# Kernel optimization log

Hardware: AMD Instinct MI355X
Metric: run time of the kernel (lower is better)

## Reference

```python
import jax, jax.numpy as jnp
import numpy as np
from jax import lax

B, C, H, W = 8, 256, 64, 64
A = 9                      # anchors per location (3 scales x 3 ratios)
STRIDE = 16
IMG = 1024                 # image_size
POST_NMS = 1000            # post_nms_top_n (also used as pre-NMS slice, as in source)
NMS_THR = 0.7
BBOX_XFORM_CLIP = 4.135166556742356  # log(1000/16)


def make_anchors():
    # ordering must match torch reshape (B,4,-1): index = a*H*W + h*W + w
    scales = jnp.array([128.0, 256.0, 512.0], dtype=jnp.float32)
    ratios = jnp.array([0.5, 1.0, 2.0], dtype=jnp.float32)
    ws = (scales[:, None] / jnp.sqrt(ratios)[None, :]).reshape(-1)  # [A]
    hs = (scales[:, None] * jnp.sqrt(ratios)[None, :]).reshape(-1)  # [A]
    cx = (jnp.arange(W, dtype=jnp.float32) + 0.5) * STRIDE
    cy = (jnp.arange(H, dtype=jnp.float32) + 0.5) * STRIDE
    cx = jnp.broadcast_to(cx[None, None, :], (A, H, W))
    cy = jnp.broadcast_to(cy[None, :, None], (A, H, W))
    aw = jnp.broadcast_to(ws[:, None, None], (A, H, W))
    ah = jnp.broadcast_to(hs[:, None, None], (A, H, W))
    anchors = jnp.stack([cx - aw / 2, cy - ah / 2, cx + aw / 2, cy + ah / 2], axis=-1)
    return anchors.reshape(-1, 4)  # [K,4] xyxy


def conv2d(x, w, b, pad):
    y = lax.conv_general_dilated(x, w, (1, 1), [(pad, pad), (pad, pad)],
                                 dimension_numbers=("NCHW", "OIHW", "NCHW"))
    return y + b[None, :, None, None]


def decode(t, anchors):
    # t: [K,4] (tx,ty,tw,th); anchors: [K,4] xyxy -> boxes xyxy
    aw = anchors[:, 2] - anchors[:, 0]
    ah = anchors[:, 3] - anchors[:, 1]
    acx = anchors[:, 0] + 0.5 * aw
    acy = anchors[:, 1] + 0.5 * ah
    cx = t[:, 0] * aw + acx
    cy = t[:, 1] * ah + acy
    w = jnp.exp(jnp.clip(t[:, 2], -BBOX_XFORM_CLIP, BBOX_XFORM_CLIP)) * aw
    h = jnp.exp(jnp.clip(t[:, 3], -BBOX_XFORM_CLIP, BBOX_XFORM_CLIP)) * ah
    return jnp.stack([cx - 0.5 * w, cy - 0.5 * h, cx + 0.5 * w, cy + 0.5 * h], axis=-1)


def box_iou(a, b):
    area_a = (a[:, 2] - a[:, 0]) * (a[:, 3] - a[:, 1])
    area_b = (b[:, 2] - b[:, 0]) * (b[:, 3] - b[:, 1])
    lt = jnp.maximum(a[:, None, :2], b[None, :, :2])
    rb = jnp.minimum(a[:, None, 2:], b[None, :, 2:])
    wh = jnp.clip(rb - lt, 0.0)
    inter = wh[..., 0] * wh[..., 1]
    return inter / (area_a[:, None] + area_b[None, :] - inter)


def filter_one(boxes, scores):
    # boxes [K,4], scores [K]. Faithful to source: torch.sort ascending,
    # slice to POST_NMS, then class-agnostic greedy NMS, pad to POST_NMS.
    order = jnp.argsort(lax.stop_gradient(scores))        # ascending (torch.sort default)
    idx = order[:POST_NMS]
    b = boxes[idx]
    s = scores[idx]
    # batched_nms internally processes boxes in descending-score order
    o2 = jnp.argsort(-lax.stop_gradient(s))
    b2 = b[o2]
    s2 = s[o2]
    iou = box_iou(b2, b2)  # [POST_NMS, POST_NMS]
    N = POST_NMS
    pos = jnp.arange(N)

    def body(i, keep):
        sup = (iou[i] > NMS_THR) & (pos > i) & keep[i]
        return keep & ~sup

    keep = lax.fori_loop(0, N, body, jnp.ones((N,), dtype=bool))
    # pack kept boxes (descending-score order) to the front, zero-pad the rest
    perm = jnp.argsort(jnp.where(keep, pos, N + pos))
    valid = pos < jnp.sum(keep)
    out_b = jnp.where(valid[:, None], b2[perm], 0.0)
    out_s = jnp.where(valid, s2[perm], 0.0)
    return out_b, out_s


def setup_inputs() -> dict:
    key = jax.random.key(0)
    ks = jax.random.split(key, 5)
    x = jax.random.normal(ks[0], (B, C, H, W), dtype=jnp.float32)
    conv_w = jax.random.normal(ks[1], (C, C, 3, 3), dtype=jnp.float32) * 0.01
    conv_b = jnp.zeros((C,), dtype=jnp.float32)
    box_w = jax.random.normal(ks[2], (4 * A, C, 1, 1), dtype=jnp.float32) * 0.01
    box_b = jnp.zeros((4 * A,), dtype=jnp.float32)
    obj_w = jax.random.normal(ks[3], (A, C, 1, 1), dtype=jnp.float32) * 0.01
    obj_b = jnp.zeros((A,), dtype=jnp.float32)
    return {"x": x, "conv_w": conv_w, "conv_b": conv_b,
            "box_w": box_w, "box_b": box_b, "obj_w": obj_w, "obj_b": obj_b}


def reference(x, conv_w, conv_b, box_w, box_b, obj_w, obj_b):
    feats = jax.nn.relu(conv2d(x, conv_w, conv_b, 1))        # [B,C,H,W]
    t = conv2d(feats, box_w, box_b, 0)                        # [B,4A,H,W]
    o = conv2d(feats, obj_w, obj_b, 0)                        # [B,A,H,W]
    t = t.reshape(B, 4, -1).transpose(0, 2, 1)                # [B,K,4]
    obj = o.reshape(B, -1)                                    # [B,K]
    anchors = make_anchors()                                  # [K,4]
    props = jax.vmap(lambda ti: decode(ti, anchors))(t)       # [B,K,4]
    props = jnp.clip(props, 0.0, float(IMG))                  # clip_boxes_to_image
    out_b, out_s = jax.vmap(filter_one)(props, obj)           # [B,POST_NMS,4],[B,POST_NMS]
    return jnp.concatenate([out_b, out_s[..., None]], axis=-1)  # [B,POST_NMS,5]
```

## Files before the change

kernel.cpp:

```cpp
#include <hip/hip_runtime.h>

#define B_ 8
#define C_ 256
#define H_ 64
#define W_ 64
#define HW_ 4096
#define HP_ 66
#define HWP_ 4224
#define A_ 9
#define SITES 36864
#define NPOST 1000
#define XCLIPF 4.1351666f
#define IMGF 1024.0f

__device__ inline unsigned keyf(float v) {
  unsigned u = __float_as_uint(v);
  return (u & 0x80000000u) ? ~u : (u | 0x80000000u);
}

__device__ __forceinline__ float dpp_shr1(float v) {
  return __int_as_float(__builtin_amdgcn_update_dpp(
      0, __float_as_int(v), 0x111 , 0xf, 0xf, true));
}
__device__ __forceinline__ float dpp_shl1(float v) {
  return __int_as_float(__builtin_amdgcn_update_dpp(
      0, __float_as_int(v), 0x101 , 0xf, 0xf, true));
}

__global__ __launch_bounds__(256) void prep(
    const float* __restrict__ x, const float* __restrict__ w,
    const float* __restrict__ box_w, const float* __restrict__ obj_w,
    float* __restrict__ xp, float* __restrict__ wq, float* __restrict__ wt) {
  int blk = blockIdx.x;
  if (blk < 8448) {
    int t = blk * 256 + threadIdx.x;
    int c4 = t & 15;
    int rr = (t >> 4) % HP_;
    int bc = t / (HP_ * 16);
    float4 v = make_float4(0.f, 0.f, 0.f, 0.f);
    if (rr >= 1 && rr <= 64)
      v = ((const float4*)x)[(size_t)bc * (HW_ / 4) + (size_t)(rr - 1) * 16 + c4];
    ((float4*)xp)[(size_t)bc * (HWP_ / 4) + (size_t)rr * 16 + c4] = v;
  } else if (blk < 8448 + 2304) {
    int idx = (blk - 8448) * 256 + threadIdx.x;
    int quad = idx / (256 * 36);
    int rem  = idx % (256 * 36);
    int ci = rem / 36;
    int k  = rem % 36;
    int q = k / 9, t = k % 9;
    wq[idx] = w[((size_t)(quad * 4 + q)) * (C_ * 9) + (size_t)ci * 9 + t];
  } else {
    int idx = (blk - 8448 - 2304) * 256 + threadIdx.x;
    if (idx < C_ * 45) {
      int ci = idx / 45, jj = idx % 45;
      wt[idx] = (jj < 36) ? box_w[(size_t)jj * C_ + ci]
                          : obj_w[(size_t)(jj - 36) * C_ + ci];
    }
  }
}

__global__ __launch_bounds__(256, 2) void conv3_4co(
    const float* __restrict__ xp, const float* __restrict__ wq,
    const float* __restrict__ bias, float* __restrict__ feats) {
#pragma clang fp contract(off)
  int b       = blockIdx.x & 7;
  int j       = blockIdx.x >> 3;
  int quad    = j & 63;
  int quarter = j >> 6;
  int co0 = quad << 2;
  int row16 = threadIdx.x >> 4;
  int chunk = threadIdx.x & 15;
  int gr = (quarter << 4) + row16;
  int c0 = chunk << 2;

  const float* px0 = xp + (size_t)b * C_ * HWP_ + (size_t)gr * W_ + c0;
  const float* wqb = wq + (size_t)quad * (C_ * 36);

  float acc[4][4][9];
#pragma unroll
  for (int q = 0; q < 4; ++q)
#pragma unroll
    for (int p = 0; p < 4; ++p)
#pragma unroll
      for (int t = 0; t < 9; ++t) acc[q][p][t] = 0.f;

#pragma unroll 2
  for (int ci = 0; ci < C_; ++ci) {
    const float* pr = px0 + (size_t)ci * HWP_;
    float4 tA = ((const float4*)(pr      ))[0];
    float4 mA = ((const float4*)(pr +  64))[0];
    float4 bA = ((const float4*)(pr + 128))[0];

    float T[6], M[6], Bo[6];
    T[1]=tA.x;  T[2]=tA.y;  T[3]=tA.z;  T[4]=tA.w;
    M[1]=mA.x;  M[2]=mA.y;  M[3]=mA.z;  M[4]=mA.w;
    Bo[1]=bA.x; Bo[2]=bA.y; Bo[3]=bA.z; Bo[4]=bA.w;

    T[0]  = dpp_shr1(T[4]);   T[5]  = dpp_shl1(T[1]);
    M[0]  = dpp_shr1(M[4]);   M[5]  = dpp_shl1(M[1]);
    Bo[0] = dpp_shr1(Bo[4]);  Bo[5] = dpp_shl1(Bo[1]);

    const float* wrow = wqb + ci * 36;
    float w9[4][9];
#pragma unroll
    for (int q = 0; q < 4; ++q)
#pragma unroll
      for (int t = 0; t < 9; ++t) w9[q][t] = wrow[q * 9 + t];

#pragma unroll
    for (int q = 0; q < 4; ++q)
#pragma unroll
      for (int p = 0; p < 4; ++p) {
        acc[q][p][0] = fmaf(w9[q][0], T[p],     acc[q][p][0]);
        acc[q][p][1] = fmaf(w9[q][1], T[p+1],   acc[q][p][1]);
        acc[q][p][2] = fmaf(w9[q][2], T[p+2],   acc[q][p][2]);
        acc[q][p][3] = fmaf(w9[q][3], M[p],     acc[q][p][3]);
        acc[q][p][4] = fmaf(w9[q][4], M[p+1],   acc[q][p][4]);
        acc[q][p][5] = fmaf(w9[q][5], M[p+2],   acc[q][p][5]);
        acc[q][p][6] = fmaf(w9[q][6], Bo[p],    acc[q][p][6]);
        acc[q][p][7] = fmaf(w9[q][7], Bo[p+1],  acc[q][p][7]);
        acc[q][p][8] = fmaf(w9[q][8], Bo[p+2],  acc[q][p][8]);
      }
  }

#pragma unroll
  for (int q = 0; q < 4; ++q) {
    float bv = bias[co0 + q];
    float ov[4];
#pragma unroll
    for (int p = 0; p < 4; ++p) {
      float a = 0.f;
#pragma unroll
      for (int t = 0; t < 9; ++t) a = a + acc[q][p][t];
      a = a + bv;
      ov[p] = a > 0.f ? a : 0.f;
    }
    float4* fo = (float4*)(feats + ((size_t)b * C_ + co0 + q) * HW_ + (size_t)gr * W_ + c0);
    fo[0] = make_float4(ov[0], ov[1], ov[2], ov[3]);
  }
}

__global__ __launch_bounds__(64) void conv1_all45(
    const float* __restrict__ feats, const float* __restrict__ wt,
    const float* __restrict__ box_b, const float* __restrict__ obj_b,
    float* __restrict__ tbox, float* __restrict__ scores) {
#pragma clang fp contract(off)
  int gidx = blockIdx.x * 64 + threadIdx.x;
  int b  = gidx >> 12;
  int hw = gidx & 4095;
  const float* f = feats + (size_t)b * C_ * HW_ + hw;
  float acc[45];
#pragma unroll
  for (int jj = 0; jj < 45; ++jj) acc[jj] = 0.f;
#pragma unroll 4
  for (int ci = 0; ci < C_; ++ci) {
    float fv = f[(size_t)ci * HW_];
    const float* wr = wt + ci * 45;
#pragma unroll
    for (int jj = 0; jj < 45; ++jj)
      acc[jj] = fmaf(wr[jj], fv, acc[jj]);
  }
#pragma unroll
  for (int c = 0; c < 36; ++c) {
    int k = c / 9, a = c - k * 9;
    tbox[(size_t)b * 4 * SITES + (size_t)k * SITES + (size_t)a * HW_ + hw] = acc[c] + box_b[c];
  }
#pragma unroll
  for (int a = 0; a < 9; ++a)
    scores[(size_t)b * SITES + (size_t)a * HW_ + hw] = acc[36 + a] + obj_b[a];
}

__global__ __launch_bounds__(1024) void select_sort_decode(
    const float* __restrict__ scores, const float* __restrict__ tbox,
    float* __restrict__ s2, float* __restrict__ b2) {
#pragma clang fp contract(off)
  int b = blockIdx.x;
  const float* s = scores + (size_t)b * SITES;
  __shared__ unsigned hist[256];
  __shared__ unsigned sh_prefix, sh_mask, sh_cless;
  __shared__ int sh_target;
  __shared__ int sh_cnt, sh_eq;
  __shared__ int sh_sel[1024];
  __shared__ int sh_eqList[4096];
  __shared__ float ss[NPOST];
  __shared__ int st[NPOST];
  if (threadIdx.x == 0) {
    sh_prefix = 0; sh_mask = 0; sh_target = NPOST - 1; sh_cless = 0;
    sh_cnt = 0; sh_eq = 0;
  }
  unsigned kreg[36];
#pragma unroll
  for (int t = 0; t < 36; ++t)
    kreg[t] = keyf(s[threadIdx.x + t * 1024]);
  for (int shift = 24; shift >= 0; shift -= 8) {
    if (threadIdx.x < 256) hist[threadIdx.x] = 0;
    __syncthreads();
    unsigned prefix = sh_prefix, mask = sh_mask;
#pragma unroll
    for (int t = 0; t < 36; ++t) {
      unsigned k = kreg[t];
      if ((k & mask) == prefix) atomicAdd(&hist[(k >> shift) & 255u], 1u);
    }
    __syncthreads();
    if (threadIdx.x == 0) {
      unsigned cum = 0; int tg = sh_target; int v = 0;
      for (; v < 256; ++v) {
        unsigned h = hist[v];
        if (cum + h > (unsigned)tg) break;
        cum += h;
      }
      sh_prefix |= ((unsigned)v) << shift;
      sh_mask   |= 0xFFu << shift;
      sh_target  = tg - (int)cum;
      sh_cless  += cum;
    }
    __syncthreads();
  }
  unsigned K = sh_prefix;
  int need = NPOST - (int)sh_cless;
#pragma unroll
  for (int t = 0; t < 36; ++t) {
    unsigned k = kreg[t];
    int i = threadIdx.x + t * 1024;
    if (k < K) {
      int pos = atomicAdd(&sh_cnt, 1);
      sh_sel[pos] = i;
    } else if (k == K) {
      int e = atomicAdd(&sh_eq, 1);
      if (e < 4096) sh_eqList[e] = i;
    }
  }
  __syncthreads();
  {
    int E = sh_eq; if (E > 4096) E = 4096;
    int base = sh_cnt;
    for (int t = threadIdx.x; t < E; t += 1024) {
      int site = sh_eqList[t];
      int rank = 0;
      for (int q = 0; q < E; ++q) rank += (sh_eqList[q] < site);
      if (rank < need) sh_sel[base + rank] = site;
    }
  }
  __syncthreads();
  for (int t = threadIdx.x; t < NPOST; t += 1024) {
    int site = sh_sel[t];
    st[t] = site;
    ss[t] = s[site];
  }
  __syncthreads();
  if (threadIdx.x < NPOST) {
    int r = threadIdx.x;
    float sr = ss[r]; int sir = st[r];
    int d = 0;
    for (int q = 0; q < NPOST; ++q) {
      float sq = ss[q];
      d += (int)((sq > sr) || (sq == sr && st[q] < sir));
    }
    s2[(size_t)b * NPOST + d] = sr;
    int site = sir;
    int a = site / HW_;
    int hw = site - a * HW_;
    int h = hw / W_, wc = hw - h * W_;
    int sidx = a / 3, ridx = a - sidx * 3;
    float scale = (sidx == 0) ? 128.f : ((sidx == 1) ? 256.f : 512.f);
    float ratio = (ridx == 0) ? 0.5f : ((ridx == 1) ? 1.0f : 2.0f);
    float sq = sqrtf(ratio);
    float wsa = scale / sq;
    float hsa = scale * sq;
    float cx = ((float)wc + 0.5f) * 16.f;
    float cy = ((float)h + 0.5f) * 16.f;
    float ax1 = cx - wsa * 0.5f;
    float ay1 = cy - hsa * 0.5f;
    float ax2 = cx + wsa * 0.5f;
    float ay2 = cy + hsa * 0.5f;
    float aw = ax2 - ax1, ah = ay2 - ay1;
    float m1 = 0.5f * aw, m2 = 0.5f * ah;
    float acx = ax1 + m1, acy = ay1 + m2;
    const float* tb = tbox + (size_t)b * 4 * SITES + site;
    float t0 = tb[0];
    float t1 = tb[SITES];
    float t2 = tb[2 * (size_t)SITES];
    float t3 = tb[3 * (size_t)SITES];
    if (t2 < -XCLIPF) t2 = -XCLIPF;
    if (t2 > XCLIPF) t2 = XCLIPF;
    if (t3 < -XCLIPF) t3 = -XCLIPF;
    if (t3 > XCLIPF) t3 = XCLIPF;
    float pm0 = t0 * aw;  float pcx = pm0 + acx;
    float pm1 = t1 * ah;  float pcy = pm1 + acy;
    float pw = expf(t2) * aw;
    float ph = expf(t3) * ah;
    float hw0 = 0.5f * pw, hh0 = 0.5f * ph;
    float x1 = pcx - hw0, y1 = pcy - hh0;
    float x2 = pcx + hw0, y2 = pcy + hh0;
    x1 = x1 < 0.f ? 0.f : (x1 > IMGF ? IMGF : x1);
    y1 = y1 < 0.f ? 0.f : (y1 > IMGF ? IMGF : y1);
    x2 = x2 < 0.f ? 0.f : (x2 > IMGF ? IMGF : x2);
    y2 = y2 < 0.f ? 0.f : (y2 > IMGF ? IMGF : y2);
    float* o = b2 + ((size_t)b * NPOST + d) * 4;
    o[0] = x1; o[1] = y1; o[2] = x2; o[3] = y2;
  }
}

__global__ __launch_bounds__(256) void mask_kernel(
    const float* __restrict__ b2, unsigned long long* __restrict__ sup) {
#pragma clang fp contract(off)
  int b = blockIdx.x / 63;
  int i0 = (blockIdx.x % 63) * 16;
  __shared__ float bs[NPOST * 4];
  __shared__ float area[NPOST];
  for (int t = threadIdx.x; t < NPOST * 4; t += 256) bs[t] = b2[(size_t)b * NPOST * 4 + t];
  __syncthreads();
  for (int t = threadIdx.x; t < NPOST; t += 256)
    area[t] = (bs[t * 4 + 2] - bs[t * 4]) * (bs[t * 4 + 3] - bs[t * 4 + 1]);
  __syncthreads();
  int i = i0 + (threadIdx.x & 15);
  int wd = threadIdx.x >> 4;
  if (i >= NPOST) return;
  float ax1 = bs[i * 4], ay1 = bs[i * 4 + 1], ax2 = bs[i * 4 + 2], ay2 = bs[i * 4 + 3];
  float aa = area[i];
  unsigned long long m = 0;
  for (int bit = 0; bit < 64; ++bit) {
    int j = wd * 64 + bit;
    if (j > i && j < NPOST) {
      float lx = fmaxf(ax1, bs[j * 4]);
      float ly = fmaxf(ay1, bs[j * 4 + 1]);
      float rx = fminf(ax2, bs[j * 4 + 2]);
      float ry = fminf(ay2, bs[j * 4 + 3]);
      float iw = rx - lx; if (iw < 0.f) iw = 0.f;
      float ih = ry - ly; if (ih < 0.f) ih = 0.f;
      float inter = iw * ih;
      float denom = (aa + area[j]) - inter;
      float iou = inter / denom;
      if (iou > 0.7f) m |= 1ull << bit;
    }
  }
  sup[((size_t)b * NPOST + i) * 16 + wd] = m;
}

__global__ __launch_bounds__(64) void nms_out(
    const unsigned long long* __restrict__ sup, const float* __restrict__ b2,
    const float* __restrict__ s2, float* __restrict__ out) {
  int b = blockIdx.x;
  int lane = threadIdx.x;
  unsigned long long kw = 0;
  if (lane < 16) kw = (lane < 15) ? ~0ull : ((1ull << 40) - 1);
  const unsigned long long* ms = sup + (size_t)b * NPOST * 16;
  unsigned long long mb[8];
#pragma unroll
  for (int k = 0; k < 8; ++k)
    mb[k] = (lane < 16) ? ms[(size_t)k * 16 + lane] : 0ull;
  for (int i0 = 0; i0 < NPOST; i0 += 8) {
    unsigned long long nb[8];
#pragma unroll
    for (int k = 0; k < 8; ++k) {
      int nx = i0 + 8 + k;
      nb[k] = (nx < NPOST && lane < 16) ? ms[(size_t)nx * 16 + lane] : 0ull;
    }
#pragma unroll
    for (int k = 0; k < 8; ++k) {
      int i = i0 + k;
      unsigned long long w = __shfl(kw, i >> 6, 64);
      if ((w >> (i & 63)) & 1ull) {
        if (lane < 16) kw &= ~mb[k];
      }
    }
#pragma unroll
    for (int k = 0; k < 8; ++k) mb[k] = nb[k];
  }
  __shared__ unsigned long long keeps[16];
  if (lane < 16) keeps[lane] = kw;
  __syncthreads();
  int total = 0;
#pragma unroll
  for (int k = 0; k < 16; ++k) total += __popcll(keeps[k]);
  for (int i = lane; i < NPOST; i += 64) {
    int w = i >> 6;
    int before = 0;
    for (int k = 0; k < w; ++k) before += __popcll(keeps[k]);
    before += __popcll(keeps[w] & ((1ull << (i & 63)) - 1));
    bool kept = (keeps[w] >> (i & 63)) & 1ull;
    if (kept) {
      size_t ob = (size_t)b * (NPOST * 5) + (size_t)before * 5;
      const float* src = b2 + ((size_t)b * NPOST + i) * 4;
      out[ob + 0] = src[0];
      out[ob + 1] = src[1];
      out[ob + 2] = src[2];
      out[ob + 3] = src[3];
      out[ob + 4] = s2[(size_t)b * NPOST + i];
    }
    if (i >= total) {
      size_t ob = (size_t)b * (NPOST * 5) + (size_t)i * 5;
      for (int c = 0; c < 5; ++c) out[ob + c] = 0.f;
    }
  }
}

extern "C" void kernel_launch(void* const* d_in, const int* in_sizes, int n_in,
                              void* d_out, int out_size, void* d_ws, size_t ws_size,
                              hipStream_t stream) {
  const float *x = nullptr, *conv_w = nullptr, *conv_b = nullptr,
              *box_w = nullptr, *box_b = nullptr, *obj_w = nullptr, *obj_b = nullptr;
  for (int i = 0; i < n_in; ++i) {
    switch (in_sizes[i]) {
      case 8388608: x = (const float*)d_in[i]; break;
      case 589824:  conv_w = (const float*)d_in[i]; break;
      case 256:     conv_b = (const float*)d_in[i]; break;
      case 9216:    box_w = (const float*)d_in[i]; break;
      case 36:      box_b = (const float*)d_in[i]; break;
      case 2304:    obj_w = (const float*)d_in[i]; break;
      case 9:       obj_b = (const float*)d_in[i]; break;
    }
  }
  float* out = (float*)d_out;

  char* p = (char*)d_ws;
  auto alloc = [&](size_t n) { char* q = p; p += (n + 255) & ~255ull; return (void*)q; };
  float* feats  = (float*)alloc((size_t)B_ * C_ * HW_ * 4);
  float* tbox   = (float*)alloc((size_t)B_ * 4 * SITES * 4);
  float* scores = (float*)alloc((size_t)B_ * SITES * 4);
  float* xpad   = (float*)alloc((size_t)B_ * C_ * HWP_ * 4);
  float* wq     = (float*)alloc((size_t)64 * C_ * 36 * 4);
  float* wt     = (float*)alloc((size_t)C_ * 45 * 4);
  float* s2     = (float*)alloc((size_t)B_ * NPOST * 4);
  float* b2     = (float*)alloc((size_t)B_ * NPOST * 4 * 4);
  unsigned long long* sup = (unsigned long long*)alloc((size_t)B_ * NPOST * 16 * 8);

  hipLaunchKernelGGL(prep, dim3(8448 + 2304 + 45), dim3(256), 0, stream,
                     x, conv_w, box_w, obj_w, xpad, wq, wt);
  hipLaunchKernelGGL(conv3_4co, dim3(B_ * 64 * 4), dim3(256), 0, stream,
                     xpad, wq, conv_b, feats);
  hipLaunchKernelGGL(conv1_all45, dim3(B_ * HW_ / 64), dim3(64), 0, stream,
                     feats, wt, box_b, obj_b, tbox, scores);
  hipLaunchKernelGGL(select_sort_decode, dim3(B_), dim3(1024), 0, stream,
                     scores, tbox, s2, b2);
  hipLaunchKernelGGL(mask_kernel, dim3(B_ * 63), dim3(256), 0, stream, b2, sup);
  hipLaunchKernelGGL(nms_out, dim3(B_), dim3(64), 0, stream, sup, b2, s2, out);
}
```

Measured before the change: 850.6 us.

## Stage padded input rows in double-buffered LDS shared across four channel quads

Restructures the 3x3 conv kernel so each block covers a 4-row band and 16 output channels, with each wavefront handling one output-channel quad. The six padded input rows per channel are staged once into a double-buffered shared-memory tile, and the next channel is prefetched while the current one is computed. The aim is to cut redundant global loads of the input, which is now read once per block and reused by four quads instead of being reloaded per quad. In exchange, a __syncthreads is added on every channel iteration, and only 96 threads do the staging, which may stall the FMA pipeline.

```diff
diff --git a/kernel.cpp b/kernel.cpp
--- a/kernel.cpp
+++ b/kernel.cpp
@@ -59,21 +59,26 @@
   }
 }
 
-__global__ __launch_bounds__(256, 2) void conv3_4co(
+__global__ __launch_bounds__(256, 2) void conv3_lds(
     const float* __restrict__ xp, const float* __restrict__ wq,
     const float* __restrict__ bias, float* __restrict__ feats) {
 #pragma clang fp contract(off)
-  int b       = blockIdx.x & 7;
-  int j       = blockIdx.x >> 3;
-  int quad    = j & 63;
-  int quarter = j >> 6;
-  int co0 = quad << 2;
-  int row16 = threadIdx.x >> 4;
-  int chunk = threadIdx.x & 15;
-  int gr = (quarter << 4) + row16;
+  int b    = blockIdx.x & 7;
+  int j    = blockIdx.x >> 3;
+  int cg   = j & 15;
+  int band = j >> 4;
+  int wid  = threadIdx.x >> 6;
+  int lane = threadIdx.x & 63;
+  int quad = cg * 4 + wid;
+  int co0  = quad << 2;
+  int wrow = lane >> 4;
+  int chunk = lane & 15;
+  int gr = band * 4 + wrow;
   int c0 = chunk << 2;
 
-  const float* px0 = xp + (size_t)b * C_ * HWP_ + (size_t)gr * W_ + c0;
+  __shared__ float xs[2][384];
+
+  const float* xb = xp + (size_t)b * C_ * HWP_ + (size_t)(band * 4) * W_;
   const float* wqb = wq + (size_t)quad * (C_ * 36);
 
   float acc[4][4][9];
@@ -83,13 +88,23 @@
     for (int p = 0; p < 4; ++p)
 #pragma unroll
       for (int t = 0; t < 9; ++t) acc[q][p][t] = 0.f;
+
+  bool stager = (threadIdx.x < 96);
+  if (stager)
+    ((float4*)xs[0])[threadIdx.x] = ((const float4*)xb)[threadIdx.x];
+  __syncthreads();
 
 #pragma unroll 2
   for (int ci = 0; ci < C_; ++ci) {
-    const float* pr = px0 + (size_t)ci * HWP_;
-    float4 tA = ((const float4*)(pr      ))[0];
-    float4 mA = ((const float4*)(pr +  64))[0];
-    float4 bA = ((const float4*)(pr + 128))[0];
+    float4 nxt;
+    bool do_stage = stager && (ci + 1 < C_);
+    if (do_stage)
+      nxt = ((const float4*)(xb + (size_t)(ci + 1) * HWP_))[threadIdx.x];
+
+    const float* xr = xs[ci & 1];
+    float4 tA = *(const float4*)&xr[(size_t)(wrow    ) * 64 + c0];
+    float4 mA = *(const float4*)&xr[(size_t)(wrow + 1) * 64 + c0];
+    float4 bA = *(const float4*)&xr[(size_t)(wrow + 2) * 64 + c0];
 
     float T[6], M[6], Bo[6];
     T[1]=tA.x;  T[2]=tA.y;  T[3]=tA.z;  T[4]=tA.w;
@@ -100,12 +115,12 @@
     M[0]  = dpp_shr1(M[4]);   M[5]  = dpp_shl1(M[1]);
     Bo[0] = dpp_shr1(Bo[4]);  Bo[5] = dpp_shl1(Bo[1]);
 
-    const float* wrow = wqb + ci * 36;
+    const float* wrp = wqb + ci * 36;
     float w9[4][9];
 #pragma unroll
     for (int q = 0; q < 4; ++q)
 #pragma unroll
-      for (int t = 0; t < 9; ++t) w9[q][t] = wrow[q * 9 + t];
+      for (int t = 0; t < 9; ++t) w9[q][t] = wrp[q * 9 + t];
 
 #pragma unroll
     for (int q = 0; q < 4; ++q)
@@ -121,6 +136,10 @@
         acc[q][p][7] = fmaf(w9[q][7], Bo[p+1],  acc[q][p][7]);
         acc[q][p][8] = fmaf(w9[q][8], Bo[p+2],  acc[q][p][8]);
       }
+
+    if (do_stage)
+      ((float4*)xs[(ci + 1) & 1])[threadIdx.x] = nxt;
+    __syncthreads();
   }
 
 #pragma unroll
@@ -427,7 +446,7 @@
 
   hipLaunchKernelGGL(prep, dim3(8448 + 2304 + 45), dim3(256), 0, stream,
                      x, conv_w, box_w, obj_w, xpad, wq, wt);
-  hipLaunchKernelGGL(conv3_4co, dim3(B_ * 64 * 4), dim3(256), 0, stream,
+  hipLaunchKernelGGL(conv3_lds, dim3(B_ * 16 * 16), dim3(256), 0, stream,
                      xpad, wq, conv_b, feats);
   hipLaunchKernelGGL(conv1_all45, dim3(B_ * HW_ / 64), dim3(64), 0, stream,
                      feats, wt, box_b, obj_b, tbox, scores);
```

Result: slower. 2.833 ms (+233.1%).
